# Performance work log

Hardware: AMD Instinct MI355X
Metric: run time of the kernel (lower is better)

The kernel has to match this reference:

```python
import jax, jax.numpy as jnp
import numpy as np

N = 4_194_304  # number of 3D point observations
M = 2048       # number of cameras


def rodrigues(r):
    """Axis-angle vectors [..., 3] -> rotation matrices [..., 3, 3] (vectorized)."""
    theta = jnp.linalg.norm(r, axis=-1, keepdims=True)          # [...,1]
    k = r / jnp.maximum(theta, 1e-12)                            # unit axis
    kx, ky, kz = k[..., 0], k[..., 1], k[..., 2]
    z = jnp.zeros_like(kx)
    K = jnp.stack([
        jnp.stack([z, -kz, ky], axis=-1),
        jnp.stack([kz, z, -kx], axis=-1),
        jnp.stack([-ky, kx, z], axis=-1),
    ], axis=-2)                                                  # [...,3,3]
    st = jnp.sin(theta)[..., None]
    ct = jnp.cos(theta)[..., None]
    I = jnp.eye(3, dtype=r.dtype)
    return I + st * K + (1.0 - ct) * (K @ K)


def setup_inputs() -> dict:
    key = jax.random.key(0)
    ks = jax.random.split(key, 8)
    X_world = jax.random.normal(ks[0], (N, 3), dtype=jnp.float32)
    camera_indices = jax.random.randint(ks[1], (N,), 0, M, dtype=jnp.int32)
    # noisy intrinsics: fx, fy ~ 1000, cx, cy ~ 500
    base_K = jnp.array([1000.0, 1000.0, 500.0, 500.0], dtype=jnp.float32)
    intrinsics_noisy = base_K + 5.0 * jax.random.normal(ks[2], (M, 4), dtype=jnp.float32)
    # noisy extrinsics: proper rotations, translation pushing points to z ~ 5
    R_noisy = rodrigues(0.5 * jax.random.normal(ks[3], (M, 3), dtype=jnp.float32))
    t_noisy = 0.1 * jax.random.normal(ks[4], (M, 3), dtype=jnp.float32) \
        + jnp.array([0.0, 0.0, 5.0], dtype=jnp.float32)
    # learned correction deltas (small, nonzero to exercise rodrigues branch)
    intrinsic_deltas = 0.01 * jax.random.normal(ks[5], (M, 4), dtype=jnp.float32)
    rotation_deltas = 0.01 * jax.random.normal(ks[6], (M, 3), dtype=jnp.float32)
    translation_deltas = 0.01 * jax.random.normal(ks[7], (M, 3), dtype=jnp.float32)
    return {
        "X_world": X_world,
        "camera_indices": camera_indices,
        "intrinsics_noisy": intrinsics_noisy,
        "R_noisy": R_noisy,
        "t_noisy": t_noisy,
        "intrinsic_deltas": intrinsic_deltas,
        "rotation_deltas": rotation_deltas,
        "translation_deltas": translation_deltas,
    }


def reference(X_world, camera_indices, intrinsics_noisy, R_noisy, t_noisy,
              intrinsic_deltas, rotation_deltas, translation_deltas):
    # Corrected per-camera parameters (computed once per camera, M small)
    R_corr = rodrigues(rotation_deltas) @ R_noisy            # [M,3,3]
    t_corr = t_noisy + translation_deltas                    # [M,3]
    K_corr = intrinsics_noisy + intrinsic_deltas             # [M,4] fx,fy,cx,cy
    # Gather per-point camera params (vectorized replacement of the python loop)
    Rg = R_corr[camera_indices]                              # [N,3,3]
    tg = t_corr[camera_indices]                              # [N,3]
    Kg = K_corr[camera_indices]                              # [N,4]
    # World -> camera, then perspective projection
    Xc = jnp.einsum('nij,nj->ni', Rg, X_world) + tg          # [N,3]
    z = Xc[:, 2]
    u = Kg[:, 0] * Xc[:, 0] / z + Kg[:, 2]
    v = Kg[:, 1] * Xc[:, 1] / z + Kg[:, 3]
    return jnp.stack([u, v], axis=-1)                        # [N,2]
```

## Files before the change

kernel.cpp:

```cpp
#include <hip/hip_runtime.h>
#include <math.h>

#define N_PTS 4194304
#define M_CAM 2048
#define NG (N_PTS / 4)
#define THREADS 1024
#define BLOCKS 256
#define GSTRIDE (THREADS * BLOCKS)


__global__ __launch_bounds__(1024) void camera_project_fused(
        const float* __restrict__ X,
        const int* __restrict__ idx,
        const float* __restrict__ intr,
        const float* __restrict__ Rn,
        const float* __restrict__ tn,
        const float* __restrict__ intr_d,
        const float* __restrict__ rot_d,
        const float* __restrict__ trans_d,
        float* __restrict__ out) {
    __shared__ float4 l0[M_CAM];
    __shared__ float4 l1[M_CAM];
    __shared__ float4 l2[M_CAM];
    __shared__ float2 lc[M_CAM];

    const int tid = blockIdx.x * THREADS + threadIdx.x;
    const float4* __restrict__ X4 = (const float4*)X;
    const int4* __restrict__ I4 = (const int4*)idx;
    float4* __restrict__ O4 = (float4*)out;

    const int g0 = tid;
    const int g1 = tid + GSTRIDE;
    const int g2 = tid + 2 * GSTRIDE;
    const int g3 = tid + 3 * GSTRIDE;

    float4 a0 = X4[3 * g0 + 0], b0 = X4[3 * g0 + 1], c0 = X4[3 * g0 + 2];
    float4 a1 = X4[3 * g1 + 0], b1 = X4[3 * g1 + 1], c1 = X4[3 * g1 + 2];
    float4 a2 = X4[3 * g2 + 0], b2 = X4[3 * g2 + 1], c2 = X4[3 * g2 + 2];
    float4 a3 = X4[3 * g3 + 0], b3 = X4[3 * g3 + 1], c3 = X4[3 * g3 + 2];
    int4 i0 = I4[g0], i1 = I4[g1], i2 = I4[g2], i3 = I4[g3];

    for (int m = threadIdx.x; m < M_CAM; m += THREADS) {
        float rx = rot_d[3 * m + 0];
        float ry = rot_d[3 * m + 1];
        float rz = rot_d[3 * m + 2];
        float theta = sqrtf(rx * rx + ry * ry + rz * rz);
        float inv = 1.0f / fmaxf(theta, 1e-12f);
        float kx = rx * inv, ky = ry * inv, kz = rz * inv;
        float st = sinf(theta);
        float ct = cosf(theta);
        float omc = 1.0f - ct;

        float Rd[9];
        Rd[0] = 1.0f - omc * (ky * ky + kz * kz);
        Rd[1] = -st * kz + omc * (kx * ky);
        Rd[2] =  st * ky + omc * (kx * kz);
        Rd[3] =  st * kz + omc * (kx * ky);
        Rd[4] = 1.0f - omc * (kx * kx + kz * kz);
        Rd[5] = -st * kx + omc * (ky * kz);
        Rd[6] = -st * ky + omc * (kx * kz);
        Rd[7] =  st * kx + omc * (ky * kz);
        Rd[8] = 1.0f - omc * (kx * kx + ky * ky);

        float Rm[9];
#pragma unroll
        for (int i = 0; i < 3; ++i) {
#pragma unroll
            for (int j = 0; j < 3; ++j) {
                Rm[3 * i + j] = Rd[3 * i + 0] * Rn[9 * m + 0 + j]
                              + Rd[3 * i + 1] * Rn[9 * m + 3 + j]
                              + Rd[3 * i + 2] * Rn[9 * m + 6 + j];
            }
        }

        float t0 = tn[3 * m + 0] + trans_d[3 * m + 0];
        float t1 = tn[3 * m + 1] + trans_d[3 * m + 1];
        float t2 = tn[3 * m + 2] + trans_d[3 * m + 2];

        const float4* intr4 = (const float4*)intr;
        const float4* intrd4 = (const float4*)intr_d;
        float4 ki = intr4[m];
        float4 kd = intrd4[m];
        float fx = ki.x + kd.x;
        float fy = ki.y + kd.y;
        float cx = ki.z + kd.z;
        float cy = ki.w + kd.w;

        l0[m] = make_float4(fx * Rm[0], fx * Rm[1], fx * Rm[2], fx * t0);
        l1[m] = make_float4(fy * Rm[3], fy * Rm[4], fy * Rm[5], fy * t1);
        l2[m] = make_float4(Rm[6], Rm[7], Rm[8], t2);
        lc[m] = make_float2(cx, cy);
    }
    __syncthreads();

    auto proj = [&](int c, float px, float py, float pz) -> float2 {
        float4 r0 = l0[c];
        float4 r1 = l1[c];
        float4 r2 = l2[c];
        float2 cc = lc[c];
        float nu = fmaf(r0.x, px, fmaf(r0.y, py, fmaf(r0.z, pz, r0.w)));
        float nv = fmaf(r1.x, px, fmaf(r1.y, py, fmaf(r1.z, pz, r1.w)));
        float zc = fmaf(r2.x, px, fmaf(r2.y, py, fmaf(r2.z, pz, r2.w)));
        float iz = 1.0f / zc;
        return make_float2(fmaf(nu, iz, cc.x), fmaf(nv, iz, cc.y));
    };

    {
        float2 u0 = proj(i0.x, a0.x, a0.y, a0.z);
        float2 u1 = proj(i0.y, a0.w, b0.x, b0.y);
        float2 u2 = proj(i0.z, b0.z, b0.w, c0.x);
        float2 u3 = proj(i0.w, c0.y, c0.z, c0.w);
        O4[2 * g0 + 0] = make_float4(u0.x, u0.y, u1.x, u1.y);
        O4[2 * g0 + 1] = make_float4(u2.x, u2.y, u3.x, u3.y);
    }
    {
        float2 u0 = proj(i1.x, a1.x, a1.y, a1.z);
        float2 u1 = proj(i1.y, a1.w, b1.x, b1.y);
        float2 u2 = proj(i1.z, b1.z, b1.w, c1.x);
        float2 u3 = proj(i1.w, c1.y, c1.z, c1.w);
        O4[2 * g1 + 0] = make_float4(u0.x, u0.y, u1.x, u1.y);
        O4[2 * g1 + 1] = make_float4(u2.x, u2.y, u3.x, u3.y);
    }
    {
        float2 u0 = proj(i2.x, a2.x, a2.y, a2.z);
        float2 u1 = proj(i2.y, a2.w, b2.x, b2.y);
        float2 u2 = proj(i2.z, b2.z, b2.w, c2.x);
        float2 u3 = proj(i2.w, c2.y, c2.z, c2.w);
        O4[2 * g2 + 0] = make_float4(u0.x, u0.y, u1.x, u1.y);
        O4[2 * g2 + 1] = make_float4(u2.x, u2.y, u3.x, u3.y);
    }
    {
        float2 u0 = proj(i3.x, a3.x, a3.y, a3.z);
        float2 u1 = proj(i3.y, a3.w, b3.x, b3.y);
        float2 u2 = proj(i3.z, b3.z, b3.w, c3.x);
        float2 u3 = proj(i3.w, c3.y, c3.z, c3.w);
        O4[2 * g3 + 0] = make_float4(u0.x, u0.y, u1.x, u1.y);
        O4[2 * g3 + 1] = make_float4(u2.x, u2.y, u3.x, u3.y);
    }
}

extern "C" void kernel_launch(void* const* d_in, const int* in_sizes, int n_in,
                              void* d_out, int out_size, void* d_ws, size_t ws_size,
                              hipStream_t stream) {
    const float* X_world      = (const float*)d_in[0];
    const int*   cam_idx      = (const int*)d_in[1];
    const float* intrinsics   = (const float*)d_in[2];
    const float* R_noisy      = (const float*)d_in[3];
    const float* t_noisy      = (const float*)d_in[4];
    const float* intr_deltas  = (const float*)d_in[5];
    const float* rot_deltas   = (const float*)d_in[6];
    const float* trans_deltas = (const float*)d_in[7];
    float* out = (float*)d_out;

    camera_project_fused<<<BLOCKS, THREADS, 0, stream>>>(
        X_world, cam_idx, intrinsics, R_noisy, t_noisy,
        intr_deltas, rot_deltas, trans_deltas, out);
}
```

Measured before the change: 27.30 us.

## Double-buffer point loads, fold principal point into camera table, prefetch camera params

Replaces the up-front load of all four point groups with a two-deep software pipeline: only the first group (and the next) are in flight, and each later load is issued while the previous group is projected. Camera parameter loads are hoisted into registers before the table build. The principal point is folded into the first two projection rows (cx*row2, cy*row2), so the shared-memory lc table and the per-point add are removed. This cuts register pressure and LDS traffic, but less load latency is exposed up front before the sync, and folding the principal point can change rounding slightly.

```diff
diff --git a/kernel.cpp b/kernel.cpp
--- a/kernel.cpp
+++ b/kernel.cpp
@@ -22,28 +22,40 @@
     __shared__ float4 l0[M_CAM];
     __shared__ float4 l1[M_CAM];
     __shared__ float4 l2[M_CAM];
-    __shared__ float2 lc[M_CAM];
 
     const int tid = blockIdx.x * THREADS + threadIdx.x;
     const float4* __restrict__ X4 = (const float4*)X;
     const int4* __restrict__ I4 = (const int4*)idx;
     float4* __restrict__ O4 = (float4*)out;
 
+    const int m0 = threadIdx.x;
+    const int m1 = threadIdx.x + THREADS;
+    const float4* intr4 = (const float4*)intr;
+    const float4* intrd4 = (const float4*)intr_d;
+
+    float rd0x = rot_d[3 * m0 + 0], rd0y = rot_d[3 * m0 + 1], rd0z = rot_d[3 * m0 + 2];
+    float rd1x = rot_d[3 * m1 + 0], rd1y = rot_d[3 * m1 + 1], rd1z = rot_d[3 * m1 + 2];
+    float Rn0[9], Rn1[9];
+#pragma unroll
+    for (int j = 0; j < 9; ++j) Rn0[j] = Rn[9 * m0 + j];
+#pragma unroll
+    for (int j = 0; j < 9; ++j) Rn1[j] = Rn[9 * m1 + j];
+    float tn0x = tn[3 * m0 + 0], tn0y = tn[3 * m0 + 1], tn0z = tn[3 * m0 + 2];
+    float tn1x = tn[3 * m1 + 0], tn1y = tn[3 * m1 + 1], tn1z = tn[3 * m1 + 2];
+    float td0x = trans_d[3 * m0 + 0], td0y = trans_d[3 * m0 + 1], td0z = trans_d[3 * m0 + 2];
+    float td1x = trans_d[3 * m1 + 0], td1y = trans_d[3 * m1 + 1], td1z = trans_d[3 * m1 + 2];
+    float4 ki0 = intr4[m0], kd0 = intrd4[m0];
+    float4 ki1 = intr4[m1], kd1 = intrd4[m1];
+
     const int g0 = tid;
-    const int g1 = tid + GSTRIDE;
-    const int g2 = tid + 2 * GSTRIDE;
-    const int g3 = tid + 3 * GSTRIDE;
+    float4 cA = X4[3 * g0 + 0];
+    float4 cB = X4[3 * g0 + 1];
+    float4 cC = X4[3 * g0 + 2];
+    int4 cI = I4[g0];
 
-    float4 a0 = X4[3 * g0 + 0], b0 = X4[3 * g0 + 1], c0 = X4[3 * g0 + 2];
-    float4 a1 = X4[3 * g1 + 0], b1 = X4[3 * g1 + 1], c1 = X4[3 * g1 + 2];
-    float4 a2 = X4[3 * g2 + 0], b2 = X4[3 * g2 + 1], c2 = X4[3 * g2 + 2];
-    float4 a3 = X4[3 * g3 + 0], b3 = X4[3 * g3 + 1], c3 = X4[3 * g3 + 2];
-    int4 i0 = I4[g0], i1 = I4[g1], i2 = I4[g2], i3 = I4[g3];
-
-    for (int m = threadIdx.x; m < M_CAM; m += THREADS) {
-        float rx = rot_d[3 * m + 0];
-        float ry = rot_d[3 * m + 1];
-        float rz = rot_d[3 * m + 2];
+    auto build = [&](int m, float rx, float ry, float rz, const float* Rnl,
+                     float tnx, float tny, float tnz,
+                     float tdx, float tdy, float tdz, float4 ki, float4 kd) {
         float theta = sqrtf(rx * rx + ry * ry + rz * rz);
         float inv = 1.0f / fmaxf(theta, 1e-12f);
         float kx = rx * inv, ky = ry * inv, kz = rz * inv;
@@ -67,76 +79,73 @@
         for (int i = 0; i < 3; ++i) {
 #pragma unroll
             for (int j = 0; j < 3; ++j) {
-                Rm[3 * i + j] = Rd[3 * i + 0] * Rn[9 * m + 0 + j]
-                              + Rd[3 * i + 1] * Rn[9 * m + 3 + j]
-                              + Rd[3 * i + 2] * Rn[9 * m + 6 + j];
+                Rm[3 * i + j] = Rd[3 * i + 0] * Rnl[0 + j]
+                              + Rd[3 * i + 1] * Rnl[3 + j]
+                              + Rd[3 * i + 2] * Rnl[6 + j];
             }
         }
 
-        float t0 = tn[3 * m + 0] + trans_d[3 * m + 0];
-        float t1 = tn[3 * m + 1] + trans_d[3 * m + 1];
-        float t2 = tn[3 * m + 2] + trans_d[3 * m + 2];
+        float t0 = tnx + tdx, t1 = tny + tdy, t2 = tnz + tdz;
+        float fx = ki.x + kd.x, fy = ki.y + kd.y;
+        float cx = ki.z + kd.z, cy = ki.w + kd.w;
 
-        const float4* intr4 = (const float4*)intr;
-        const float4* intrd4 = (const float4*)intr_d;
-        float4 ki = intr4[m];
-        float4 kd = intrd4[m];
-        float fx = ki.x + kd.x;
-        float fy = ki.y + kd.y;
-        float cx = ki.z + kd.z;
-        float cy = ki.w + kd.w;
-
-        l0[m] = make_float4(fx * Rm[0], fx * Rm[1], fx * Rm[2], fx * t0);
-        l1[m] = make_float4(fy * Rm[3], fy * Rm[4], fy * Rm[5], fy * t1);
+        l0[m] = make_float4(fmaf(fx, Rm[0], cx * Rm[6]),
+                            fmaf(fx, Rm[1], cx * Rm[7]),
+                            fmaf(fx, Rm[2], cx * Rm[8]),
+                            fmaf(fx, t0, cx * t2));
+        l1[m] = make_float4(fmaf(fy, Rm[3], cy * Rm[6]),
+                            fmaf(fy, Rm[4], cy * Rm[7]),
+                            fmaf(fy, Rm[5], cy * Rm[8]),
+                            fmaf(fy, t1, cy * t2));
         l2[m] = make_float4(Rm[6], Rm[7], Rm[8], t2);
-        lc[m] = make_float2(cx, cy);
-    }
+    };
+    build(m0, rd0x, rd0y, rd0z, Rn0, tn0x, tn0y, tn0z, td0x, td0y, td0z, ki0, kd0);
+    build(m1, rd1x, rd1y, rd1z, Rn1, tn1x, tn1y, tn1z, td1x, td1y, td1z, ki1, kd1);
     __syncthreads();
 
     auto proj = [&](int c, float px, float py, float pz) -> float2 {
         float4 r0 = l0[c];
         float4 r1 = l1[c];
         float4 r2 = l2[c];
-        float2 cc = lc[c];
         float nu = fmaf(r0.x, px, fmaf(r0.y, py, fmaf(r0.z, pz, r0.w)));
         float nv = fmaf(r1.x, px, fmaf(r1.y, py, fmaf(r1.z, pz, r1.w)));
         float zc = fmaf(r2.x, px, fmaf(r2.y, py, fmaf(r2.z, pz, r2.w)));
         float iz = 1.0f / zc;
-        return make_float2(fmaf(nu, iz, cc.x), fmaf(nv, iz, cc.y));
+        return make_float2(nu * iz, nv * iz);
+    };
+    auto process = [&](int g, float4 a, float4 b, float4 c, int4 ci) {
+        float2 u0 = proj(ci.x, a.x, a.y, a.z);
+        float2 u1 = proj(ci.y, a.w, b.x, b.y);
+        float2 u2 = proj(ci.z, b.z, b.w, c.x);
+        float2 u3 = proj(ci.w, c.y, c.z, c.w);
+        O4[2 * g + 0] = make_float4(u0.x, u0.y, u1.x, u1.y);
+        O4[2 * g + 1] = make_float4(u2.x, u2.y, u3.x, u3.y);
     };
 
-    {
-        float2 u0 = proj(i0.x, a0.x, a0.y, a0.z);
-        float2 u1 = proj(i0.y, a0.w, b0.x, b0.y);
-        float2 u2 = proj(i0.z, b0.z, b0.w, c0.x);
-        float2 u3 = proj(i0.w, c0.y, c0.z, c0.w);
-        O4[2 * g0 + 0] = make_float4(u0.x, u0.y, u1.x, u1.y);
-        O4[2 * g0 + 1] = make_float4(u2.x, u2.y, u3.x, u3.y);
-    }
-    {
-        float2 u0 = proj(i1.x, a1.x, a1.y, a1.z);
-        float2 u1 = proj(i1.y, a1.w, b1.x, b1.y);
-        float2 u2 = proj(i1.z, b1.z, b1.w, c1.x);
-        float2 u3 = proj(i1.w, c1.y, c1.z, c1.w);
-        O4[2 * g1 + 0] = make_float4(u0.x, u0.y, u1.x, u1.y);
-        O4[2 * g1 + 1] = make_float4(u2.x, u2.y, u3.x, u3.y);
-    }
-    {
-        float2 u0 = proj(i2.x, a2.x, a2.y, a2.z);
-        float2 u1 = proj(i2.y, a2.w, b2.x, b2.y);
-        float2 u2 = proj(i2.z, b2.z, b2.w, c2.x);
-        float2 u3 = proj(i2.w, c2.y, c2.z, c2.w);
-        O4[2 * g2 + 0] = make_float4(u0.x, u0.y, u1.x, u1.y);
-        O4[2 * g2 + 1] = make_float4(u2.x, u2.y, u3.x, u3.y);
-    }
-    {
-        float2 u0 = proj(i3.x, a3.x, a3.y, a3.z);
-        float2 u1 = proj(i3.y, a3.w, b3.x, b3.y);
-        float2 u2 = proj(i3.z, b3.z, b3.w, c3.x);
-        float2 u3 = proj(i3.w, c3.y, c3.z, c3.w);
-        O4[2 * g3 + 0] = make_float4(u0.x, u0.y, u1.x, u1.y);
-        O4[2 * g3 + 1] = make_float4(u2.x, u2.y, u3.x, u3.y);
-    }
+    const int g1 = g0 + GSTRIDE;
+    float4 nA = X4[3 * g1 + 0];
+    float4 nB = X4[3 * g1 + 1];
+    float4 nC = X4[3 * g1 + 2];
+    int4 nI = I4[g1];
+
+    process(g0, cA, cB, cC, cI);
+
+    const int g2 = g0 + 2 * GSTRIDE;
+    cA = X4[3 * g2 + 0];
+    cB = X4[3 * g2 + 1];
+    cC = X4[3 * g2 + 2];
+    cI = I4[g2];
+
+    process(g1, nA, nB, nC, nI);
+
+    const int g3 = g0 + 3 * GSTRIDE;
+    nA = X4[3 * g3 + 0];
+    nB = X4[3 * g3 + 1];
+    nC = X4[3 * g3 + 2];
+    nI = I4[g3];
+
+    process(g2, cA, cB, cC, cI);
+    process(g3, nA, nB, nC, nI);
 }
 
 extern "C" void kernel_launch(void* const* d_in, const int* in_sizes, int n_in,
```

Measured after the change: 22.48 us. -17.7%, faster.
